# Kernel optimization log

Hardware: AMD Instinct MI355X
Metric: run time of the kernel (lower is better)

## Reference

```python
import jax, jax.numpy as jnp
import numpy as np

N_NODES = 100000
N_EDGES = 1600000
IN_DIM, HID_DIM, OUT_DIM = 128, 128, 64


def setup_inputs() -> dict:
    key = jax.random.key(0)
    k1, k2, k3, k4 = jax.random.split(key, 4)
    x = jax.random.normal(k1, (N_NODES, IN_DIM), dtype=jnp.float32)
    edge_index = jax.random.randint(k2, (2, N_EDGES), 0, N_NODES, dtype=jnp.int64)
    # Glorot-ish init for weights, zeros for biases (as in PyG GCNConv defaults)
    W1 = jax.random.normal(k3, (IN_DIM, HID_DIM), dtype=jnp.float32) * (1.0 / np.sqrt(IN_DIM))
    b1 = jnp.zeros((HID_DIM,), dtype=jnp.float32)
    W2 = jax.random.normal(k4, (HID_DIM, OUT_DIM), dtype=jnp.float32) * (1.0 / np.sqrt(HID_DIM))
    b2 = jnp.zeros((OUT_DIM,), dtype=jnp.float32)
    return {"x": x, "edge_index": edge_index, "W1": W1, "b1": b1, "W2": W2, "b2": b2}


def _build_norm(edge_index, num_nodes):
    """Add self-loops and compute symmetric GCN normalization per edge.
    Returns (src, dst, norm) with self-loops appended."""
    loops = jnp.arange(num_nodes, dtype=edge_index.dtype)
    src = jnp.concatenate([edge_index[0], loops])
    dst = jnpp_concat = jnp.concatenate([edge_index[1], loops])
    deg = jax.ops.segment_sum(jnp.ones_like(dst, dtype=jnp.float32), dst,
                              num_segments=num_nodes)
    dinv = jax.lax.rsqrt(deg)  # deg >= 1 due to self-loops
    norm = dinv[src] * dinv[dst]  # [E + N]
    return src, dst, norm


def _gcn_conv(h, W, b, src, dst, norm, num_nodes):
    h = h @ W                                   # [N, F_out]
    msg = h[src] * norm[:, None]                # gather + scale, [E+N, F_out]
    agg = jax.ops.segment_sum(msg, dst, num_segments=num_nodes)
    return agg + b


def reference(x, edge_index, W1, b1, W2, b2):
    num_nodes = x.shape[0]
    src, dst, norm = _build_norm(edge_index, num_nodes)
    h = jax.nn.relu(_gcn_conv(x, W1, b1, src, dst, norm, num_nodes))
    return _gcn_conv(h, W2, b2, src, dst, norm, num_nodes)
```

## Files before the change

### kernel.cpp

```cpp
#include <hip/hip_runtime.h>

#define NN 100000
#define NE 1600000
#define NB 782
#define NBPAD 1024
#define CAPB 3072
#define EPB 8192
#define BFT 1024
#define NBF ((NE + EPB - 1) / EPB)
#define NCAST2 ((NN * 32 + 1023) / 1024)
#define NPREP2 16
#define NROWPAD 100096
#define DPAD 136
#define OPAD 72
#define MAXE 64

typedef __attribute__((ext_vector_type(8))) short short8;
typedef __attribute__((ext_vector_type(4))) float f32x4;

__device__ __forceinline__ unsigned short bf16rn(float f) {
    unsigned u = __float_as_uint(f);
    return (unsigned short)((u + 0x7FFFu + ((u >> 16) & 1u)) >> 16);
}
__device__ __forceinline__ float4 bf2x4(uint2 g) {
    float4 r;
    r.x = __uint_as_float(g.x << 16);
    r.y = __uint_as_float(g.x & 0xFFFF0000u);
    r.z = __uint_as_float(g.y << 16);
    r.w = __uint_as_float(g.y & 0xFFFF0000u);
    return r;
}
__device__ __forceinline__ uint2 packbf4(float4 v) {
    uint2 u;
    u.x = (unsigned)bf16rn(v.x) | ((unsigned)bf16rn(v.y) << 16);
    u.y = (unsigned)bf16rn(v.z) | ((unsigned)bf16rn(v.w) << 16);
    return u;
}
__device__ __forceinline__ void acc4(float4& a, uint2 v, float q) {
    a.x = fmaf(__uint_as_float(v.x << 16), q, a.x);
    a.y = fmaf(__uint_as_float(v.x & 0xFFFF0000u), q, a.y);
    a.z = fmaf(__uint_as_float(v.y << 16), q, a.z);
    a.w = fmaf(__uint_as_float(v.y & 0xFFFF0000u), q, a.w);
}
__device__ __forceinline__ float decq(unsigned e) {
    return __uint_as_float(0x38000000u | ((e & 0x7FFFu) << 12));
}
__device__ __forceinline__ int xcd_swz(int bid, int nwg) {
    int q = nwg >> 3, r = nwg & 7;
    int x = bid & 7, j = bid >> 3;
    int base = (x < r) ? x * (q + 1) : r * (q + 1) + (x - r) * q;
    return base + j;
}

__device__ __forceinline__ int load_node(const void* ei, int i64, long long idx) {
    return i64 ? (int)((const long long*)ei)[idx] : ((const int*)ei)[idx];
}

__global__ __launch_bounds__(1024) void front_k(const void* __restrict__ ei,
                                                int* __restrict__ cur,
                                                unsigned* __restrict__ bstage,
                                                const float* __restrict__ x,
                                                ushort* __restrict__ xb,
                                                const float* __restrict__ W1,
                                                const float* __restrict__ W2,
                                                ushort* __restrict__ W1t,
                                                ushort* __restrict__ W2t) {
    __shared__ unsigned binned[EPB];
    __shared__ int lcnt[NBPAD];
    __shared__ int lpos[NBPAD];
    __shared__ int gbase[NBPAD];
    __shared__ int tsum[NBPAD];
    __shared__ int i64sh;
    int bid = blockIdx.x;
    int tid = threadIdx.x;

    if (bid >= NBF) {
        int cb = bid - NBF;
        if (cb < NCAST2) {
            long long i = (long long)cb * 1024 + tid;
            if (i < (long long)NN * 32)
                ((uint2*)xb)[i] = packbf4(((const float4*)x)[i]);
        } else {
            int i = (cb - NCAST2) * 1024 + tid;
            if (i < 128 * 128) {
                int k = i >> 7, n = i & 127;
                W1t[n * 128 + k] = bf16rn(W1[k * 128 + n]);
            }
            if (i < 128 * 64) {
                int k = i >> 6, n = i & 63;
                W2t[n * 128 + k] = bf16rn(W2[k * 64 + n]);
            }
        }
        return;
    }

    long long e0 = (long long)bid * EPB;

    if (tid < 64) {
        unsigned w = ((const unsigned*)ei)[2 * tid + 1];
        unsigned long long b = __ballot(w == 0u);
        if (tid == 0) i64sh = (b == 0xFFFFFFFFFFFFFFFFull) ? 1 : 0;
    }
    lcnt[tid] = 0;
    __syncthreads();
    int i64 = i64sh;

    for (int i = tid; i < EPB; i += BFT) {
        long long e = e0 + i;
        if (e < NE) {
            int d = load_node(ei, i64, (long long)NE + e);
            atomicAdd(&lcnt[d >> 7], 1);
        }
    }
    __syncthreads();

    int c = lcnt[tid];
    tsum[tid] = c;
    __syncthreads();
    for (int off = 1; off < NBPAD; off <<= 1) {
        int v = (tid >= off) ? tsum[tid - off] : 0;
        __syncthreads();
        tsum[tid] += v;
        __syncthreads();
    }
    int excl = tsum[tid] - c;
    lcnt[tid] = excl;
    lpos[tid] = excl;
    if (tid < NB) gbase[tid] = c ? atomicAdd(&cur[tid], c) : 0;
    __syncthreads();

    for (int i = tid; i < EPB; i += BFT) {
        long long e = e0 + i;
        if (e < NE) {
            int sv = load_node(ei, i64, e);
            int d  = load_node(ei, i64, (long long)NE + e);
            int b  = d >> 7;
            int p  = atomicAdd(&lpos[b], 1);
            binned[p] = ((unsigned)(d & 127) << 17) | (unsigned)sv;
        }
    }
    __syncthreads();

    if (tid < NB) {
        int start = lcnt[tid], endp = lpos[tid];
        int gb = gbase[tid];
        unsigned* dst = bstage + (long long)tid * CAPB;
        for (int k = start; k < endp; k++) {
            int go = gb + (k - start);
            if (go < CAPB) dst[go] = binned[k];
        }
    }
}

__global__ __launch_bounds__(256) void regroup_k(const int* __restrict__ cur,
                                                 const unsigned* __restrict__ bstage,
                                                 int* __restrict__ cnt,
                                                 int* __restrict__ rowstart,
                                                 unsigned* __restrict__ grouped,
                                                 float* __restrict__ dinv) {
    __shared__ unsigned stash[CAPB];
    __shared__ unsigned srt[CAPB];
    __shared__ int lcnt[128], lofs[128], lpos[128], sc[128];
    int tid = threadIdx.x;
    int b = blockIdx.x;

    int total = cur[b];
    if (total > CAPB) total = CAPB;
    const unsigned* seg = bstage + (long long)b * CAPB;
    for (int i = tid; i < total; i += 256) stash[i] = seg[i];
    __syncthreads();

    if (tid < 128) { lcnt[tid] = 0; lpos[tid] = 0; }
    __syncthreads();
    for (int i = tid; i < total; i += 256)
        atomicAdd(&lcnt[stash[i] >> 17], 1);
    __syncthreads();

    if (tid < 128) sc[tid] = lcnt[tid];
    __syncthreads();
    for (int off = 1; off < 128; off <<= 1) {
        int v = 0;
        if (tid < 128 && tid >= off) v = sc[tid - off];
        __syncthreads();
        if (tid < 128) sc[tid] += v;
        __syncthreads();
    }
    if (tid < 128) {
        lofs[tid] = sc[tid] - lcnt[tid];
        int node = b * 128 + tid;
        if (node < NN) {
            cnt[node] = lcnt[tid];
            rowstart[node] = b * CAPB + lofs[tid];
            dinv[node] = rsqrtf((float)(lcnt[tid] + 1));
        }
    }
    __syncthreads();

    for (int i = tid; i < total; i += 256) {
        unsigned e = stash[i];
        int nl = e >> 17;
        int p = atomicAdd(&lpos[nl], 1);
        srt[lofs[nl] + p] = e;
    }
    __syncthreads();

    unsigned* g = grouped + (long long)b * CAPB;
    for (int i = tid; i < total; i += 256) g[i] = srt[i] & 0x1FFFFu;
}

__global__ __launch_bounds__(256) void qn2_k(const int* __restrict__ cur,
                                             const float* __restrict__ dinv,
                                             unsigned* __restrict__ grouped) {
    int b = blockIdx.x;
    int total = cur[b];
    if (total > CAPB) total = CAPB;
    unsigned* g = grouped + (long long)b * CAPB;
    for (int i = threadIdx.x; i < total; i += 256) {
        unsigned s = g[i];
        unsigned bits = __float_as_uint(dinv[s]);
        g[i] = (s << 15) | ((bits >> 12) & 0x7FFFu);
    }
}

template <int LPN, bool BIAS, bool OUTB>
__global__ __launch_bounds__(256) void pull6_k(const unsigned* __restrict__ grouped,
                                               const int* __restrict__ rowstart,
                                               const int* __restrict__ cnt,
                                               const float* __restrict__ dinv,
                                               const ushort* __restrict__ hb,
                                               const float* __restrict__ bias,
                                               void* __restrict__ out) {
    __shared__ unsigned ed[256 / LPN][MAXE];
    int tid = threadIdx.x;
    int nib = tid / LPN;
    int lane = tid & (LPN - 1);
    int node = xcd_swz(blockIdx.x, (int)gridDim.x) * (256 / LPN) + nib;
    if (node >= NN) return;

    const uint2* h2 = (const uint2*)hb;
    float di = dinv[node];
    float w0 = di * di;
    float4 A = make_float4(0.f, 0.f, 0.f, 0.f);
    float4 B = make_float4(0.f, 0.f, 0.f, 0.f);
    {
        float4 hv = bf2x4(h2[(unsigned)node * LPN + lane]);
        A.x = hv.x * w0; A.y = hv.y * w0; A.z = hv.z * w0; A.w = hv.w * w0;
    }

    int deg = cnt[node];
    const unsigned* row = grouped + rowstart[node];
    int s = deg < MAXE ? deg : MAXE;

    for (int t = lane; t < s; t += LPN) ed[nib][t] = row[t];

    int j = 0;
    if (s >= 8) {
        uint2 v[8];
        float q[8];
#pragma unroll
        for (int t = 0; t < 8; t++) {
            unsigned e = ed[nib][t];
            q[t] = decq(e) * di;
            v[t] = h2[(e >> 15) * LPN + lane];
        }
        for (; j + 16 <= s; j += 8) {
#pragma unroll
            for (int t = 0; t < 8; t++) {
                unsigned e = ed[nib][j + 8 + t];
                uint2 nv = h2[(e >> 15) * LPN + lane];
                if (t & 1) acc4(B, v[t], q[t]);
                else       acc4(A, v[t], q[t]);
                v[t] = nv; q[t] = decq(e) * di;
            }
        }
#pragma unroll
        for (int t = 0; t < 8; t++) {
            if (t & 1) acc4(B, v[t], q[t]);
            else       acc4(A, v[t], q[t]);
        }
        j += 8;
    }
    for (; j < s; j++) {
        unsigned e = ed[nib][j];
        uint2 v0 = h2[(e >> 15) * LPN + lane];
        acc4(A, v0, decq(e) * di);
    }
    for (; j < deg; j++) {
        unsigned e = row[j];
        uint2 v0 = h2[(e >> 15) * LPN + lane];
        acc4(A, v0, decq(e) * di);
    }

    float4 o;
    o.x = A.x + B.x; o.y = A.y + B.y; o.z = A.z + B.z; o.w = A.w + B.w;
    if (BIAS) {
        float4 bb = ((const float4*)bias)[lane];
        o.x += bb.x; o.y += bb.y; o.z += bb.z; o.w += bb.w;
    }
    if (OUTB)
        ((uint2*)out)[(unsigned)node * LPN + lane] = packbf4(o);
    else
        ((float4*)out)[(unsigned)node * LPN + lane] = o;
}

__global__ __launch_bounds__(256) void dgemm_mfma_k(const ushort* __restrict__ Ab,
                                                    const ushort* __restrict__ W1t,
                                                    const float* __restrict__ b1,
                                                    const ushort* __restrict__ W2t,
                                                    ushort* __restrict__ H2b) {
    __shared__ ushort Tt[4][32 * DPAD];
    __shared__ ushort Ot[4][32 * OPAD];
    int tid = threadIdx.x;
    int wv = tid >> 6, lane = tid & 63;
    int m16 = lane & 15, quad = lane >> 4;
    int row0 = blockIdx.x * 128 + wv * 32;

    short8 af[2][4];
#pragma unroll
    for (int mt = 0; mt < 2; mt++)
#pragma unroll
        for (int kc = 0; kc < 4; kc++)
            af[mt][kc] = *(const short8*)(Ab + (long long)(row0 + mt * 16 + m16) * 128
                                          + kc * 32 + quad * 8);
    f32x4 accA[2][8];
#pragma unroll
    for (int mt = 0; mt < 2; mt++)
#pragma unroll
        for (int nt = 0; nt < 8; nt++) accA[mt][nt] = (f32x4){0.f, 0.f, 0.f, 0.f};

#pragma unroll
    for (int nt = 0; nt < 8; nt++) {
#pragma unroll
        for (int kc = 0; kc < 4; kc++) {
            short8 bf = *(const short8*)(W1t + (nt * 16 + m16) * 128 + kc * 32 + quad * 8);
            accA[0][nt] = __builtin_amdgcn_mfma_f32_16x16x32_bf16(af[0][kc], bf, accA[0][nt], 0, 0, 0);
            accA[1][nt] = __builtin_amdgcn_mfma_f32_16x16x32_bf16(af[1][kc], bf, accA[1][nt], 0, 0, 0);
        }
    }

#pragma unroll
    for (int nt = 0; nt < 8; nt++) {
        float bb = b1[nt * 16 + m16];
#pragma unroll
        for (int mt = 0; mt < 2; mt++)
#pragma unroll
            for (int r = 0; r < 4; r++) {
                float v = fmaxf(accA[mt][nt][r] + bb, 0.f);
                Tt[wv][(mt * 16 + quad * 4 + r) * DPAD + nt * 16 + m16] = bf16rn(v);
            }
    }
    __syncthreads();

    f32x4 accB[2][4];
#pragma unroll
    for (int mt = 0; mt < 2; mt++)
#pragma unroll
        for (int nt = 0; nt < 4; nt++) accB[mt][nt] = (f32x4){0.f, 0.f, 0.f, 0.f};

#pragma unroll
    for (int nt = 0; nt < 4; nt++) {
#pragma unroll
        for (int kc = 0; kc < 4; kc++) {
            short8 bf = *(const short8*)(W2t + (nt * 16 + m16) * 128 + kc * 32 + quad * 8);
#pragma unroll
            for (int mt = 0; mt < 2; mt++) {
                short8 aT = *(const short8*)(&Tt[wv][(mt * 16 + m16) * DPAD + kc * 32 + quad * 8]);
                accB[mt][nt] = __builtin_amdgcn_mfma_f32_16x16x32_bf16(aT, bf, accB[mt][nt], 0, 0, 0);
            }
        }
    }

#pragma unroll
    for (int nt = 0; nt < 4; nt++)
#pragma unroll
        for (int mt = 0; mt < 2; mt++)
#pragma unroll
            for (int r = 0; r < 4; r++)
                Ot[wv][(mt * 16 + quad * 4 + r) * OPAD + nt * 16 + m16] = bf16rn(accB[mt][nt][r]);
    __syncthreads();

    uint4* H4 = (uint4*)H2b;
#pragma unroll
    for (int it = 0; it < 4; it++) {
        int idx = it * 64 + lane;
        int r = idx >> 3, c = idx & 7;
        int grow = row0 + r;
        if (grow < NN) {
            uint4 v = *(const uint4*)(&Ot[wv][r * OPAD + c * 8]);
            H4[(long long)grow * 8 + c] = v;
        }
    }
}

extern "C" void kernel_launch(void* const* d_in, const int* in_sizes, int n_in,
                              void* d_out, int out_size, void* d_ws, size_t ws_size,
                              hipStream_t stream) {
    const float* x  = (const float*)d_in[0];
    const void*  ei = d_in[1];
    const float* W1 = (const float*)d_in[2];
    const float* b1 = (const float*)d_in[3];
    const float* W2 = (const float*)d_in[4];
    const float* b2 = (const float*)d_in[5];
    float* out = (float*)d_out;
    char* ws = (char*)d_ws;

    int*      cur      = (int*)(ws + 0x1000);
    int*      cnt      = (int*)(ws + 0x10000);
    int*      rowstart = (int*)(ws + 0x80000);
    unsigned* bstage   = (unsigned*)(ws + 0x100000);
    unsigned* grouped  = (unsigned*)(ws + 0xB00000);
    ushort*   xb       = (ushort*)(ws + 0x1500000);
    ushort*   aggxb    = (ushort*)(ws + 0x2F00000);
    ushort*   h2b      = (ushort*)(ws + 0x4800000);
    ushort*   W1t      = (ushort*)(ws + 0x5500000);
    ushort*   W2t      = (ushort*)(ws + 0x5510000);
    float*    dinv     = (float*)(ws + 0x5520000);

    hipMemsetAsync(cur, 0, NB * sizeof(int), stream);

    front_k<<<NBF + NCAST2 + NPREP2, BFT, 0, stream>>>(ei, cur, bstage,
                                                       x, xb, W1, W2, W1t, W2t);

    regroup_k<<<NB, 256, 0, stream>>>(cur, bstage, cnt, rowstart, grouped, dinv);
    qn2_k<<<NB, 256, 0, stream>>>(cur, dinv, grouped);

    pull6_k<32, false, true><<<(NN + 7) / 8, 256, 0, stream>>>(grouped, rowstart, cnt, dinv,
                                                               xb, nullptr, aggxb);
    dgemm_mfma_k<<<NROWPAD / 128, 256, 0, stream>>>(aggxb, W1t, b1, W2t, h2b);

    pull6_k<16, true, false><<<(NN + 15) / 16, 256, 0, stream>>>(grouped, rowstart, cnt, dinv,
                                                                 h2b, b2, out);
}
```

Measured before the change: 268.1 us.

## Fuse first-layer aggregation with both dense GEMMs into one kernel

Merges the layer-1 neighbour aggregation (pull) with the two MFMA GEMMs into a single 512-thread kernel that handles 16 nodes per block. Aggregated rows stay in shared memory and feed the W1 GEMM, ReLU and W2 GEMM directly, so the bf16 aggregated-feature buffer is no longer written to and read back from global memory, and one launch is removed. In exchange, each block runs only one 16-row MFMA tile, reloads the weight fragments from global memory per block, and adds two extra block barriers. Half the waves sit idle during the second GEMM.

```diff
diff --git a/kernel.cpp b/kernel.cpp
--- a/kernel.cpp
+++ b/kernel.cpp
@@ -10,7 +10,6 @@
 #define NBF ((NE + EPB - 1) / EPB)
 #define NCAST2 ((NN * 32 + 1023) / 1024)
 #define NPREP2 16
-#define NROWPAD 100096
 #define DPAD 136
 #define OPAD 72
 #define MAXE 64
@@ -222,6 +221,125 @@
     }
 }
 
+__global__ __launch_bounds__(512) void pullgemm_k(const unsigned* __restrict__ grouped,
+                                                  const int* __restrict__ rowstart,
+                                                  const int* __restrict__ cnt,
+                                                  const float* __restrict__ dinv,
+                                                  const ushort* __restrict__ hb,
+                                                  const ushort* __restrict__ W1t,
+                                                  const float* __restrict__ b1,
+                                                  const ushort* __restrict__ W2t,
+                                                  ushort* __restrict__ H2b) {
+    __shared__ unsigned ed[16][MAXE];
+    __shared__ ushort T1[16 * DPAD];
+    __shared__ ushort T2[16 * DPAD];
+    __shared__ ushort Ot[16 * OPAD];
+    int tid = threadIdx.x;
+    int nib = tid >> 5;
+    int lane = tid & 31;
+    int blk = xcd_swz(blockIdx.x, (int)gridDim.x);
+    int node = blk * 16 + nib;
+
+    const uint2* h2 = (const uint2*)hb;
+    float di = dinv[node];
+    float w0 = di * di;
+    float4 A = make_float4(0.f, 0.f, 0.f, 0.f);
+    float4 B = make_float4(0.f, 0.f, 0.f, 0.f);
+    {
+        float4 hv = bf2x4(h2[(unsigned)node * 32 + lane]);
+        A.x = hv.x * w0; A.y = hv.y * w0; A.z = hv.z * w0; A.w = hv.w * w0;
+    }
+
+    int deg = cnt[node];
+    const unsigned* row = grouped + rowstart[node];
+    int s = deg < MAXE ? deg : MAXE;
+
+    for (int t = lane; t < s; t += 32) ed[nib][t] = row[t];
+
+    int j = 0;
+    if (s >= 8) {
+        uint2 v[8];
+        float q[8];
+#pragma unroll
+        for (int t = 0; t < 8; t++) {
+            unsigned e = ed[nib][t];
+            q[t] = decq(e) * di;
+            v[t] = h2[(e >> 15) * 32 + lane];
+        }
+        for (; j + 16 <= s; j += 8) {
+#pragma unroll
+            for (int t = 0; t < 8; t++) {
+                unsigned e = ed[nib][j + 8 + t];
+                uint2 nv = h2[(e >> 15) * 32 + lane];
+                if (t & 1) acc4(B, v[t], q[t]);
+                else       acc4(A, v[t], q[t]);
+                v[t] = nv; q[t] = decq(e) * di;
+            }
+        }
+#pragma unroll
+        for (int t = 0; t < 8; t++) {
+            if (t & 1) acc4(B, v[t], q[t]);
+            else       acc4(A, v[t], q[t]);
+        }
+        j += 8;
+    }
+    for (; j < s; j++) {
+        unsigned e = ed[nib][j];
+        uint2 v0 = h2[(e >> 15) * 32 + lane];
+        acc4(A, v0, decq(e) * di);
+    }
+    for (; j < deg; j++) {
+        unsigned e = row[j];
+        uint2 v0 = h2[(e >> 15) * 32 + lane];
+        acc4(A, v0, decq(e) * di);
+    }
+
+    float4 o;
+    o.x = A.x + B.x; o.y = A.y + B.y; o.z = A.z + B.z; o.w = A.w + B.w;
+    ((uint2*)T1)[nib * 34 + lane] = packbf4(o);
+    __syncthreads();
+
+    int wv = tid >> 6, l64 = tid & 63;
+    int m16 = l64 & 15, quad = l64 >> 4;
+
+    f32x4 accA = (f32x4){0.f, 0.f, 0.f, 0.f};
+#pragma unroll
+    for (int kc = 0; kc < 4; kc++) {
+        short8 aT = *(const short8*)(T1 + m16 * DPAD + kc * 32 + quad * 8);
+        short8 bf = *(const short8*)(W1t + (wv * 16 + m16) * 128 + kc * 32 + quad * 8);
+        accA = __builtin_amdgcn_mfma_f32_16x16x32_bf16(aT, bf, accA, 0, 0, 0);
+    }
+    {
+        float bb = b1[wv * 16 + m16];
+#pragma unroll
+        for (int r = 0; r < 4; r++) {
+            float v = fmaxf(accA[r] + bb, 0.f);
+            T2[(quad * 4 + r) * DPAD + wv * 16 + m16] = bf16rn(v);
+        }
+    }
+    __syncthreads();
+
+    if (wv < 4) {
+        f32x4 accB = (f32x4){0.f, 0.f, 0.f, 0.f};
+#pragma unroll
+        for (int kc = 0; kc < 4; kc++) {
+            short8 aT = *(const short8*)(T2 + m16 * DPAD + kc * 32 + quad * 8);
+            short8 bf = *(const short8*)(W2t + (wv * 16 + m16) * 128 + kc * 32 + quad * 8);
+            accB = __builtin_amdgcn_mfma_f32_16x16x32_bf16(aT, bf, accB, 0, 0, 0);
+        }
+#pragma unroll
+        for (int r = 0; r < 4; r++)
+            Ot[(quad * 4 + r) * OPAD + wv * 16 + m16] = bf16rn(accB[r]);
+    }
+    __syncthreads();
+
+    if (tid < 128) {
+        int r = tid >> 3, c = tid & 7;
+        ((uint4*)H2b)[(long long)(blk * 16 + r) * 8 + c] =
+            *(const uint4*)(&Ot[r * OPAD + c * 8]);
+    }
+}
+
 template <int LPN, bool BIAS, bool OUTB>
 __global__ __launch_bounds__(256) void pull6_k(const unsigned* __restrict__ grouped,
                                                const int* __restrict__ rowstart,
@@ -303,95 +421,6 @@
         ((float4*)out)[(unsigned)node * LPN + lane] = o;
 }
 
-__global__ __launch_bounds__(256) void dgemm_mfma_k(const ushort* __restrict__ Ab,
-                                                    const ushort* __restrict__ W1t,
-                                                    const float* __restrict__ b1,
-                                                    const ushort* __restrict__ W2t,
-                                                    ushort* __restrict__ H2b) {
-    __shared__ ushort Tt[4][32 * DPAD];
-    __shared__ ushort Ot[4][32 * OPAD];
-    int tid = threadIdx.x;
-    int wv = tid >> 6, lane = tid & 63;
-    int m16 = lane & 15, quad = lane >> 4;
-    int row0 = blockIdx.x * 128 + wv * 32;
-
-    short8 af[2][4];
-#pragma unroll
-    for (int mt = 0; mt < 2; mt++)
-#pragma unroll
-        for (int kc = 0; kc < 4; kc++)
-            af[mt][kc] = *(const short8*)(Ab + (long long)(row0 + mt * 16 + m16) * 128
-                                          + kc * 32 + quad * 8);
-    f32x4 accA[2][8];
-#pragma unroll
-    for (int mt = 0; mt < 2; mt++)
-#pragma unroll
-        for (int nt = 0; nt < 8; nt++) accA[mt][nt] = (f32x4){0.f, 0.f, 0.f, 0.f};
-
-#pragma unroll
-    for (int nt = 0; nt < 8; nt++) {
-#pragma unroll
-        for (int kc = 0; kc < 4; kc++) {
-            short8 bf = *(const short8*)(W1t + (nt * 16 + m16) * 128 + kc * 32 + quad * 8);
-            accA[0][nt] = __builtin_amdgcn_mfma_f32_16x16x32_bf16(af[0][kc], bf, accA[0][nt], 0, 0, 0);
-            accA[1][nt] = __builtin_amdgcn_mfma_f32_16x16x32_bf16(af[1][kc], bf, accA[1][nt], 0, 0, 0);
-        }
-    }
-
-#pragma unroll
-    for (int nt = 0; nt < 8; nt++) {
-        float bb = b1[nt * 16 + m16];
-#pragma unroll
-        for (int mt = 0; mt < 2; mt++)
-#pragma unroll
-            for (int r = 0; r < 4; r++) {
-                float v = fmaxf(accA[mt][nt][r] + bb, 0.f);
-                Tt[wv][(mt * 16 + quad * 4 + r) * DPAD + nt * 16 + m16] = bf16rn(v);
-            }
-    }
-    __syncthreads();
-
-    f32x4 accB[2][4];
-#pragma unroll
-    for (int mt = 0; mt < 2; mt++)
-#pragma unroll
-        for (int nt = 0; nt < 4; nt++) accB[mt][nt] = (f32x4){0.f, 0.f, 0.f, 0.f};
-
-#pragma unroll
-    for (int nt = 0; nt < 4; nt++) {
-#pragma unroll
-        for (int kc = 0; kc < 4; kc++) {
-            short8 bf = *(const short8*)(W2t + (nt * 16 + m16) * 128 + kc * 32 + quad * 8);
-#pragma unroll
-            for (int mt = 0; mt < 2; mt++) {
-                short8 aT = *(const short8*)(&Tt[wv][(mt * 16 + m16) * DPAD + kc * 32 + quad * 8]);
-                accB[mt][nt] = __builtin_amdgcn_mfma_f32_16x16x32_bf16(aT, bf, accB[mt][nt], 0, 0, 0);
-            }
-        }
-    }
-
-#pragma unroll
-    for (int nt = 0; nt < 4; nt++)
-#pragma unroll
-        for (int mt = 0; mt < 2; mt++)
-#pragma unroll
-            for (int r = 0; r < 4; r++)
-                Ot[wv][(mt * 16 + quad * 4 + r) * OPAD + nt * 16 + m16] = bf16rn(accB[mt][nt][r]);
-    __syncthreads();
-
-    uint4* H4 = (uint4*)H2b;
-#pragma unroll
-    for (int it = 0; it < 4; it++) {
-        int idx = it * 64 + lane;
-        int r = idx >> 3, c = idx & 7;
-        int grow = row0 + r;
-        if (grow < NN) {
-            uint4 v = *(const uint4*)(&Ot[wv][r * OPAD + c * 8]);
-            H4[(long long)grow * 8 + c] = v;
-        }
-    }
-}
-
 extern "C" void kernel_launch(void* const* d_in, const int* in_sizes, int n_in,
                               void* d_out, int out_size, void* d_ws, size_t ws_size,
                               hipStream_t stream) {
@@ -410,7 +439,6 @@
     unsigned* bstage   = (unsigned*)(ws + 0x100000);
     unsigned* grouped  = (unsigned*)(ws + 0xB00000);
     ushort*   xb       = (ushort*)(ws + 0x1500000);
-    ushort*   aggxb    = (ushort*)(ws + 0x2F00000);
     ushort*   h2b      = (ushort*)(ws + 0x4800000);
     ushort*   W1t      = (ushort*)(ws + 0x5500000);
     ushort*   W2t      = (ushort*)(ws + 0x5510000);
@@ -424,9 +452,8 @@
     regroup_k<<<NB, 256, 0, stream>>>(cur, bstage, cnt, rowstart, grouped, dinv);
     qn2_k<<<NB, 256, 0, stream>>>(cur, dinv, grouped);
 
-    pull6_k<32, false, true><<<(NN + 7) / 8, 256, 0, stream>>>(grouped, rowstart, cnt, dinv,
-                                                               xb, nullptr, aggxb);
-    dgemm_mfma_k<<<NROWPAD / 128, 256, 0, stream>>>(aggxb, W1t, b1, W2t, h2b);
+    pullgemm_k<<<NN / 16, 512, 0, stream>>>(grouped, rowstart, cnt, dinv,
+                                            xb, W1t, b1, W2t, h2b);
 
     pull6_k<16, true, false><<<(NN + 15) / 16, 256, 0, stream>>>(grouped, rowstart, cnt, dinv,
                                                                  h2b, b2, out);
```

Result: no change. 268.3 us (+0.1%).
